# Kernel optimization log

Hardware: AMD Instinct MI355X
Metric: run time of the kernel (lower is better)

Reference implementation:

```python
import jax, jax.numpy as jnp
import numpy as np

T, H, E, I, K = 2048, 2048, 16, 512, 2
ROUTED_SCALE = 1.5   # config.moe_router_scaling_factor
SWIGLU_LIMIT = 7.0   # config.swiglu_limits[layer_id]


def setup_inputs() -> dict:
    key = jax.random.key(0)
    k1, k2, k3, k4, k5 = jax.random.split(key, 5)
    hidden_states = jax.random.normal(k1, (T, H), jnp.float32)
    gate_w = jax.random.normal(k2, (E, H), jnp.float32) * 0.02
    router_bias = jax.random.normal(k3, (E,), jnp.float32) * 0.01
    w13 = jax.random.normal(k4, (E, 2 * I, H), jnp.float32) * 0.02  # [gate; up] fused
    w2 = jax.random.normal(k5, (E, H, I), jnp.float32) * 0.02
    return {"hidden_states": hidden_states, "gate_w": gate_w,
            "router_bias": router_bias, "w13": w13, "w2": w2, "top_k": K}


def reference(hidden_states, gate_w, router_bias, w13, w2, top_k):
    n_tok = hidden_states.shape[0]
    n_exp = gate_w.shape[0]
    # fp32 gate (need_fp32_gate=True)
    router_logits = hidden_states.astype(jnp.float32) @ gate_w.T          # [T, E]
    scores = jax.nn.sigmoid(router_logits)
    # correction bias only affects expert choice, not the combine weights
    _, topk_ids = jax.lax.top_k(scores + router_bias[None, :], top_k)     # [T, K]
    topk_w = jnp.take_along_axis(scores, topk_ids, axis=1)                # [T, K]
    topk_w = topk_w / jnp.sum(topk_w, axis=1, keepdims=True)              # renormalize
    topk_w = topk_w * ROUTED_SCALE
    # scatter routing weights into dense per-expert combine weights [T, E]
    comb = jnp.zeros((n_tok, n_exp), jnp.float32)
    comb = comb.at[jnp.arange(n_tok)[:, None], topk_ids].add(topk_w)
    # expert SwiGLU MLPs, dense over experts (zero combine weight == not routed)
    gu = jnp.einsum('th,eoh->teo', hidden_states, w13)                    # [T, E, 2I]
    g, u = jnp.split(gu, 2, axis=-1)
    g = jnp.minimum(g, SWIGLU_LIMIT)                                      # gemm1_clamp_limit
    u = jnp.clip(u, -SWIGLU_LIMIT, SWIGLU_LIMIT)
    act = g * jax.nn.sigmoid(g) * u                                       # silu(gate) * up
    expert_out = jnp.einsum('tei,ehi->teh', act, w2)                      # [T, E, H]
    return jnp.einsum('teh,te->th', expert_out, comb)                     # [T, H]
```

## Files before the change

kernel.cpp:

```cpp
#include <hip/hip_runtime.h>
#include <hip/hip_bf16.h>
#include <math.h>

#define T_TOK 2048
#define H_DIM 2048
#define E_EXP 16
#define I_DIM 512
#define TWO_I 1024
#define ROUTED_SCALE 1.5f
#define SWIGLU_LIMIT 7.0f

#define BM 128
#define KC 64
#define MAX_TILES 48
#define PADMAX 6144

typedef __attribute__((ext_vector_type(8))) short bf16x8;
typedef __attribute__((ext_vector_type(4))) float f32x4;
typedef unsigned short u16;

__device__ inline u16 f2bf(float f) {
    return __builtin_bit_cast(u16, __float2bfloat16(f));
}
__device__ inline bf16x8 pack8(float4 a, float4 b) {
    bf16x8 v;
    v[0] = (short)f2bf(a.x); v[1] = (short)f2bf(a.y);
    v[2] = (short)f2bf(a.z); v[3] = (short)f2bf(a.w);
    v[4] = (short)f2bf(b.x); v[5] = (short)f2bf(b.y);
    v[6] = (short)f2bf(b.z); v[7] = (short)f2bf(b.w);
    return v;
}
__device__ inline ushort4 pack4(float4 a) {
    ushort4 v;
    v.x = f2bf(a.x); v.y = f2bf(a.y); v.z = f2bf(a.z); v.w = f2bf(a.w);
    return v;
}

__device__ inline void gload16(const u16* g, u16* l) {
    __builtin_amdgcn_global_load_lds(
        (const __attribute__((address_space(1))) void*)(g),
        (__attribute__((address_space(3))) void*)(l), 16, 0, 0);
}

#define SWZ(row, k) ((row) * 64 + ((k) ^ (((row) & 7) << 3)))

__global__ __launch_bounds__(256) void router_kernel(
    const float* __restrict__ hs, const float* __restrict__ gw,
    const float* __restrict__ bias, int* cnt, int* tok_list, float* w_list,
    u16* __restrict__ hs_bf)
{
    int wave = threadIdx.x >> 6;
    int lane = threadIdx.x & 63;
    int t = blockIdx.x * 4 + wave;
    if (t >= T_TOK) return;
    const float* x = hs + (size_t)t * H_DIM;

    float acc[E_EXP];
#pragma unroll
    for (int e = 0; e < E_EXP; ++e) acc[e] = 0.f;

#pragma unroll 2
    for (int c = 0; c < 8; ++c) {
        int col = c * 256 + lane * 4;
        float4 xv = *(const float4*)(x + col);
        *(ushort4*)(hs_bf + (size_t)t * H_DIM + col) = pack4(xv);
#pragma unroll
        for (int e = 0; e < E_EXP; ++e) {
            float4 gv = *(const float4*)(gw + (size_t)e * H_DIM + col);
            acc[e] = fmaf(xv.x, gv.x, acc[e]);
            acc[e] = fmaf(xv.y, gv.y, acc[e]);
            acc[e] = fmaf(xv.z, gv.z, acc[e]);
            acc[e] = fmaf(xv.w, gv.w, acc[e]);
        }
    }
#pragma unroll
    for (int e = 0; e < E_EXP; ++e) {
        for (int m = 32; m >= 1; m >>= 1)
            acc[e] += __shfl_xor(acc[e], m, 64);
    }
    if (lane == 0) {
        float sc[E_EXP], bsc[E_EXP];
#pragma unroll
        for (int e = 0; e < E_EXP; ++e) {
            sc[e] = 1.f / (1.f + expf(-acc[e]));
            bsc[e] = sc[e] + bias[e];
        }
        int e0 = 0; float b0 = bsc[0];
#pragma unroll
        for (int e = 1; e < E_EXP; ++e) if (bsc[e] > b0) { b0 = bsc[e]; e0 = e; }
        int e1 = -1; float b1 = -1e30f;
#pragma unroll
        for (int e = 0; e < E_EXP; ++e) {
            if (e == e0) continue;
            if (bsc[e] > b1) { b1 = bsc[e]; e1 = e; }
        }
        float s0 = sc[e0], s1 = sc[e1];
        float inv = ROUTED_SCALE / (s0 + s1);
        int p0 = atomicAdd(&cnt[e0], 1);
        tok_list[e0 * T_TOK + p0] = t;
        w_list[e0 * T_TOK + p0] = s0 * inv;
        int p1 = atomicAdd(&cnt[e1], 1);
        tok_list[e1 * T_TOK + p1] = t;
        w_list[e1 * T_TOK + p1] = s1 * inv;
    }
}

__global__ void scatter_build(const int* __restrict__ cnt,
    const int* __restrict__ tok_list, const float* __restrict__ w_list,
    int* A_tok, float* A_w, int* tile_e, int* tile_r0)
{
    int c[E_EXP], offs[E_EXP + 1];
    offs[0] = 0;
#pragma unroll
    for (int e = 0; e < E_EXP; ++e) {
        c[e] = cnt[e];
        offs[e + 1] = offs[e] + ((c[e] + BM - 1) & ~(BM - 1));
    }
    int idx = blockIdx.x * 256 + threadIdx.x;
    int e = idx >> 11;
    int pos = idx & (T_TOK - 1);
    int ce = c[e];
    int pe = (ce + BM - 1) & ~(BM - 1);
    if (pos < ce) {
        A_tok[offs[e] + pos] = tok_list[idx];
        A_w[offs[e] + pos] = w_list[idx];
    } else if (pos < pe) {
        A_tok[offs[e] + pos] = -1;
        A_w[offs[e] + pos] = 0.f;
    }
    if (idx == 0) {
        int nt = 0;
        for (int ee = 0; ee < E_EXP; ++ee) {
            int ntile = (c[ee] + BM - 1) >> 7;
            for (int j = 0; j < ntile; ++j) {
                tile_e[nt] = ee;
                tile_r0[nt] = offs[ee] + j * BM;
                ++nt;
            }
        }
        for (; nt < MAX_TILES; ++nt) tile_e[nt] = -1;
    }
}

__global__ __launch_bounds__(256, 2) void gemm1_act(
    const u16* __restrict__ hs_bf, const float* __restrict__ w13,
    const int* __restrict__ A_tok, const int* __restrict__ tile_e,
    const int* __restrict__ tile_r0, u16* __restrict__ act)
{
    int b = blockIdx.x;
    int id = (b & 7) * MAX_TILES + (b >> 3);
    int tile = id % MAX_TILES;
    int y = id / MAX_TILES;
    int e = tile_e[tile];
    if (e < 0) return;
    int row0 = tile_r0[tile];
    int i0 = y * 64;
    int tid = threadIdx.x;

    __shared__ u16 Xs[2][8192];
    __shared__ u16 Gs[2][4096];
    __shared__ u16 Us[2][4096];

    const int l = tid & 63, w = tid >> 6;

    const int rlo = l >> 3;
    const int c8 = (l & 7) << 3;
    const int ksrc = c8 ^ (rlo << 3);
    const u16* sX[4];
#pragma unroll
    for (int j = 0; j < 4; ++j) {
        int row = w * 32 + j * 8 + rlo;
        int tk = A_tok[row0 + row]; if (tk < 0) tk = 0;
        sX[j] = hs_bf + (size_t)tk * H_DIM + ksrc;
    }
    const int dX = w * 2048;

#define X_STAGE(bb, t) do { int ko = (t) * KC; \
    gload16(sX[0] + ko, &Xs[bb][dX]); \
    gload16(sX[1] + ko, &Xs[bb][dX + 512]); \
    gload16(sX[2] + ko, &Xs[bb][dX + 1024]); \
    gload16(sX[3] + ko, &Xs[bb][dX + 1536]); } while (0)

    const int srow = tid >> 2;
    const int c2 = tid & 3;
    const float* gsrc = w13 + ((size_t)e * TWO_I + i0 + srow) * H_DIM + c2 * 16;
    const float* usrc = gsrc + (size_t)I_DIM * H_DIM;
    const int wbA = SWZ(srow, c2 * 16);
    const int wbB = SWZ(srow, c2 * 16 + 8);

    float4 ga0, ga1, gb0, gb1, ua0, ua1, ub0, ub1;
#define W_LOAD(t) do { int k0 = (t) * KC; \
    ga0 = *(const float4*)(gsrc + k0);      ga1 = *(const float4*)(gsrc + k0 + 4); \
    gb0 = *(const float4*)(gsrc + k0 + 8);  gb1 = *(const float4*)(gsrc + k0 + 12); \
    ua0 = *(const float4*)(usrc + k0);      ua1 = *(const float4*)(usrc + k0 + 4); \
    ub0 = *(const float4*)(usrc + k0 + 8);  ub1 = *(const float4*)(usrc + k0 + 12); } while (0)

#define W_WRITE(bb) do { \
    *(bf16x8*)&Gs[bb][wbA] = pack8(ga0, ga1); \
    *(bf16x8*)&Gs[bb][wbB] = pack8(gb0, gb1); \
    *(bf16x8*)&Us[bb][wbA] = pack8(ua0, ua1); \
    *(bf16x8*)&Us[bb][wbB] = pack8(ub0, ub1); } while (0)

    const int wm = w >> 1, wn = w & 1;
    const int lr = l & 15, lg = l >> 4;
    int ia[4][2], ib[2][2];
#pragma unroll
    for (int kh = 0; kh < 2; ++kh) {
        int e2 = kh * 32 + lg * 8;
#pragma unroll
        for (int m = 0; m < 4; ++m) ia[m][kh] = SWZ(wm * 64 + m * 16 + lr, e2);
#pragma unroll
        for (int n = 0; n < 2; ++n) ib[n][kh] = SWZ(wn * 32 + n * 16 + lr, e2);
    }

    const f32x4 Z4 = {0.f, 0.f, 0.f, 0.f};
    f32x4 aG[4][2], aU[4][2];
#pragma unroll
    for (int m = 0; m < 4; ++m)
#pragma unroll
        for (int n = 0; n < 2; ++n) { aG[m][n] = Z4; aU[m][n] = Z4; }

    W_LOAD(0);
    X_STAGE(0, 0);
    W_WRITE(0);
    __syncthreads();
    int cur = 0;
    const int NT = H_DIM / KC;
    for (int t = 0; t < NT; ++t) {
        const bool more = (t + 1 < NT);
        if (more) {
            X_STAGE(cur ^ 1, t + 1);
            W_LOAD(t + 1);
            __builtin_amdgcn_sched_barrier(0);
        }
#pragma unroll
        for (int kh = 0; kh < 2; ++kh) {
            bf16x8 a0 = *(const bf16x8*)&Xs[cur][ia[0][kh]];
            bf16x8 a1 = *(const bf16x8*)&Xs[cur][ia[1][kh]];
            bf16x8 a2 = *(const bf16x8*)&Xs[cur][ia[2][kh]];
            bf16x8 a3 = *(const bf16x8*)&Xs[cur][ia[3][kh]];
            bf16x8 g0 = *(const bf16x8*)&Gs[cur][ib[0][kh]];
            bf16x8 g1 = *(const bf16x8*)&Gs[cur][ib[1][kh]];
            bf16x8 u0 = *(const bf16x8*)&Us[cur][ib[0][kh]];
            bf16x8 u1 = *(const bf16x8*)&Us[cur][ib[1][kh]];
            aG[0][0] = __builtin_amdgcn_mfma_f32_16x16x32_bf16(a0, g0, aG[0][0], 0, 0, 0);
            aG[0][1] = __builtin_amdgcn_mfma_f32_16x16x32_bf16(a0, g1, aG[0][1], 0, 0, 0);
            aG[1][0] = __builtin_amdgcn_mfma_f32_16x16x32_bf16(a1, g0, aG[1][0], 0, 0, 0);
            aG[1][1] = __builtin_amdgcn_mfma_f32_16x16x32_bf16(a1, g1, aG[1][1], 0, 0, 0);
            aG[2][0] = __builtin_amdgcn_mfma_f32_16x16x32_bf16(a2, g0, aG[2][0], 0, 0, 0);
            aG[2][1] = __builtin_amdgcn_mfma_f32_16x16x32_bf16(a2, g1, aG[2][1], 0, 0, 0);
            aG[3][0] = __builtin_amdgcn_mfma_f32_16x16x32_bf16(a3, g0, aG[3][0], 0, 0, 0);
            aG[3][1] = __builtin_amdgcn_mfma_f32_16x16x32_bf16(a3, g1, aG[3][1], 0, 0, 0);
            aU[0][0] = __builtin_amdgcn_mfma_f32_16x16x32_bf16(a0, u0, aU[0][0], 0, 0, 0);
            aU[0][1] = __builtin_amdgcn_mfma_f32_16x16x32_bf16(a0, u1, aU[0][1], 0, 0, 0);
            aU[1][0] = __builtin_amdgcn_mfma_f32_16x16x32_bf16(a1, u0, aU[1][0], 0, 0, 0);
            aU[1][1] = __builtin_amdgcn_mfma_f32_16x16x32_bf16(a1, u1, aU[1][1], 0, 0, 0);
            aU[2][0] = __builtin_amdgcn_mfma_f32_16x16x32_bf16(a2, u0, aU[2][0], 0, 0, 0);
            aU[2][1] = __builtin_amdgcn_mfma_f32_16x16x32_bf16(a2, u1, aU[2][1], 0, 0, 0);
            aU[3][0] = __builtin_amdgcn_mfma_f32_16x16x32_bf16(a3, u0, aU[3][0], 0, 0, 0);
            aU[3][1] = __builtin_amdgcn_mfma_f32_16x16x32_bf16(a3, u1, aU[3][1], 0, 0, 0);
        }
        if (more) W_WRITE(cur ^ 1);
        __syncthreads();
        cur ^= 1;
    }
#undef X_STAGE
#undef W_LOAD
#undef W_WRITE

#pragma unroll
    for (int m = 0; m < 4; ++m)
#pragma unroll
        for (int n = 0; n < 2; ++n) {
            int col = i0 + wn * 32 + n * 16 + lr;
            int rbase = row0 + wm * 64 + m * 16 + lg * 4;
#pragma unroll
            for (int q = 0; q < 4; ++q) {
                float g = fminf(aG[m][n][q], SWIGLU_LIMIT);
                float u = fminf(fmaxf(aU[m][n][q], -SWIGLU_LIMIT), SWIGLU_LIMIT);
                float s = 1.f / (1.f + __expf(-g));
                act[(size_t)(rbase + q) * I_DIM + col] = f2bf(g * s * u);
            }
        }
}

__global__ __launch_bounds__(256, 3) void gemm2_scatter(
    const u16* __restrict__ act, const float* __restrict__ w2,
    const int* __restrict__ A_tok, const float* __restrict__ A_w,
    const int* __restrict__ tile_e, const int* __restrict__ tile_r0,
    float* __restrict__ out)
{
    int b = blockIdx.x;
    int id = (b & 7) * 192 + (b >> 3);
    int tile = id % MAX_TILES;
    int y = id / MAX_TILES;
    int e = tile_e[tile];
    if (e < 0) return;
    int row0 = tile_r0[tile];
    int h0 = y * 64;
    int tid = threadIdx.x;

    __shared__ u16 As[2][8192];
    __shared__ u16 Bs[2][4096];
    __shared__ int toks[BM];
    __shared__ float wts[BM];
    if (tid < BM) { toks[tid] = A_tok[row0 + tid]; wts[tid] = A_w[row0 + tid]; }

    const int l = tid & 63, w = tid >> 6;

    const int rlo = l >> 3;
    const int c8 = (l & 7) << 3;
    const int ksrc = c8 ^ (rlo << 3);
    const u16* sA[4];
#pragma unroll
    for (int j = 0; j < 4; ++j) {
        int row = w * 32 + j * 8 + rlo;
        sA[j] = act + (size_t)(row0 + row) * I_DIM + ksrc;
    }
    const int dA = w * 2048;

#define A_STAGE(bb, t) do { int ko = (t) * KC; \
    gload16(sA[0] + ko, &As[bb][dA]); \
    gload16(sA[1] + ko, &As[bb][dA + 512]); \
    gload16(sA[2] + ko, &As[bb][dA + 1024]); \
    gload16(sA[3] + ko, &As[bb][dA + 1536]); } while (0)

    const int srow = tid >> 2;
    const int c2 = tid & 3;
    const float* bsrc = w2 + ((size_t)e * H_DIM + h0 + srow) * I_DIM + c2 * 16;
    const int wbA = SWZ(srow, c2 * 16);
    const int wbB = SWZ(srow, c2 * 16 + 8);

    float4 ba0, ba1, bb0, bb1;
#define B_LOAD(t) do { int k0 = (t) * KC; \
    ba0 = *(const float4*)(bsrc + k0);      ba1 = *(const float4*)(bsrc + k0 + 4); \
    bb0 = *(const float4*)(bsrc + k0 + 8);  bb1 = *(const float4*)(bsrc + k0 + 12); } while (0)

#define B_WRITE(bb) do { \
    *(bf16x8*)&Bs[bb][wbA] = pack8(ba0, ba1); \
    *(bf16x8*)&Bs[bb][wbB] = pack8(bb0, bb1); } while (0)

    const int wm = w >> 1, wn = w & 1;
    const int lr = l & 15, lg = l >> 4;
    int ia[4][2], ib[2][2];
#pragma unroll
    for (int kh = 0; kh < 2; ++kh) {
        int e2 = kh * 32 + lg * 8;
#pragma unroll
        for (int m = 0; m < 4; ++m) ia[m][kh] = SWZ(wm * 64 + m * 16 + lr, e2);
#pragma unroll
        for (int n = 0; n < 2; ++n) ib[n][kh] = SWZ(wn * 32 + n * 16 + lr, e2);
    }

    const f32x4 Z4 = {0.f, 0.f, 0.f, 0.f};
    f32x4 acc[4][2];
#pragma unroll
    for (int m = 0; m < 4; ++m)
#pragma unroll
        for (int n = 0; n < 2; ++n) acc[m][n] = Z4;

    B_LOAD(0);
    A_STAGE(0, 0);
    B_WRITE(0);
    __syncthreads();
    int cur = 0;
    const int NT = I_DIM / KC;
    for (int t = 0; t < NT; ++t) {
        const bool more = (t + 1 < NT);
        if (more) {
            A_STAGE(cur ^ 1, t + 1);
            B_LOAD(t + 1);
            __builtin_amdgcn_sched_barrier(0);
        }
#pragma unroll
        for (int kh = 0; kh < 2; ++kh) {
            bf16x8 a0 = *(const bf16x8*)&As[cur][ia[0][kh]];
            bf16x8 a1 = *(const bf16x8*)&As[cur][ia[1][kh]];
            bf16x8 a2 = *(const bf16x8*)&As[cur][ia[2][kh]];
            bf16x8 a3 = *(const bf16x8*)&As[cur][ia[3][kh]];
            bf16x8 b0 = *(const bf16x8*)&Bs[cur][ib[0][kh]];
            bf16x8 b1 = *(const bf16x8*)&Bs[cur][ib[1][kh]];
            acc[0][0] = __builtin_amdgcn_mfma_f32_16x16x32_bf16(a0, b0, acc[0][0], 0, 0, 0);
            acc[0][1] = __builtin_amdgcn_mfma_f32_16x16x32_bf16(a0, b1, acc[0][1], 0, 0, 0);
            acc[1][0] = __builtin_amdgcn_mfma_f32_16x16x32_bf16(a1, b0, acc[1][0], 0, 0, 0);
            acc[1][1] = __builtin_amdgcn_mfma_f32_16x16x32_bf16(a1, b1, acc[1][1], 0, 0, 0);
            acc[2][0] = __builtin_amdgcn_mfma_f32_16x16x32_bf16(a2, b0, acc[2][0], 0, 0, 0);
            acc[2][1] = __builtin_amdgcn_mfma_f32_16x16x32_bf16(a2, b1, acc[2][1], 0, 0, 0);
            acc[3][0] = __builtin_amdgcn_mfma_f32_16x16x32_bf16(a3, b0, acc[3][0], 0, 0, 0);
            acc[3][1] = __builtin_amdgcn_mfma_f32_16x16x32_bf16(a3, b1, acc[3][1], 0, 0, 0);
        }
        if (more) B_WRITE(cur ^ 1);
        __syncthreads();
        cur ^= 1;
    }
#undef A_STAGE
#undef B_LOAD
#undef B_WRITE

#pragma unroll
    for (int m = 0; m < 4; ++m)
#pragma unroll
        for (int n = 0; n < 2; ++n) {
            int col = h0 + wn * 32 + n * 16 + lr;
            int sbase = wm * 64 + m * 16 + lg * 4;
#pragma unroll
            for (int q = 0; q < 4; ++q) {
                int slot = sbase + q;
                int tok = toks[slot];
                if (tok >= 0)
                    atomicAdd(&out[(size_t)tok * H_DIM + col], acc[m][n][q] * wts[slot]);
            }
        }
}

extern "C" void kernel_launch(void* const* d_in, const int* in_sizes, int n_in,
                              void* d_out, int out_size, void* d_ws, size_t ws_size,
                              hipStream_t stream) {
    const float* hs   = (const float*)d_in[0];
    const float* gw   = (const float*)d_in[1];
    const float* bias = (const float*)d_in[2];
    const float* w13  = (const float*)d_in[3];
    const float* w2   = (const float*)d_in[4];
    float* out = (float*)d_out;

    char* ws = (char*)d_ws;
    int*   cnt      = (int*)(ws + 0);
    int*   tile_e   = (int*)(ws + 64);
    int*   tile_r0  = (int*)(ws + 320);
    int*   tok_list = (int*)(ws + 1024);
    float* w_list   = (float*)(ws + 132096);
    int*   A_tok    = (int*)(ws + 263168);
    float* A_w      = (float*)(ws + 287744);
    u16*   act      = (u16*)(ws + 315392);
    u16*   hs_bf    = (u16*)(ws + 6606848);

    hipMemsetAsync(d_out, 0, (size_t)T_TOK * H_DIM * sizeof(float), stream);
    hipMemsetAsync(cnt, 0, 64, stream);

    router_kernel<<<T_TOK / 4, 256, 0, stream>>>(hs, gw, bias, cnt, tok_list, w_list, hs_bf);
    scatter_build<<<(E_EXP * T_TOK) / 256, 256, 0, stream>>>(cnt, tok_list, w_list, A_tok, A_w, tile_e, tile_r0);

    gemm1_act<<<MAX_TILES * 8, 256, 0, stream>>>(hs_bf, w13, A_tok, tile_e, tile_r0, act);
    gemm2_scatter<<<MAX_TILES * 32, 256, 0, stream>>>(act, w2, A_tok, A_w, tile_e, tile_r0, out);
}
```

Baseline: 178.9 us.

## Stream fp32 weights directly into LDS via async loads and convert at MFMA read

Both expert GEMMs now bring the fp32 weight tiles into shared memory with global_load_lds instead of register loads followed by a bf16 pack and LDS store, and convert to bf16 when fragments are read. The K chunk is halved to 32 so the fp32 tiles fit, swizzles are redone, and the pipeline uses explicit vmcnt waits and raw barriers with two stages in flight. Launch-bound occupancy hints are raised, and gemm2 reads token ids and weights from global memory in the epilogue instead of shared memory. This removes register staging and VGPR pressure, at the cost of more loop iterations, more barriers, and duplicated conversion work across waves.

```diff
diff --git a/kernel.cpp b/kernel.cpp
--- a/kernel.cpp
+++ b/kernel.cpp
@@ -11,9 +11,8 @@
 #define SWIGLU_LIMIT 7.0f
 
 #define BM 128
-#define KC 64
+#define KC 32
 #define MAX_TILES 48
-#define PADMAX 6144
 
 typedef __attribute__((ext_vector_type(8))) short bf16x8;
 typedef __attribute__((ext_vector_type(4))) float f32x4;
@@ -21,28 +20,36 @@
 
 __device__ inline u16 f2bf(float f) {
     return __builtin_bit_cast(u16, __float2bfloat16(f));
-}
-__device__ inline bf16x8 pack8(float4 a, float4 b) {
-    bf16x8 v;
-    v[0] = (short)f2bf(a.x); v[1] = (short)f2bf(a.y);
-    v[2] = (short)f2bf(a.z); v[3] = (short)f2bf(a.w);
-    v[4] = (short)f2bf(b.x); v[5] = (short)f2bf(b.y);
-    v[6] = (short)f2bf(b.z); v[7] = (short)f2bf(b.w);
-    return v;
 }
 __device__ inline ushort4 pack4(float4 a) {
     ushort4 v;
     v.x = f2bf(a.x); v.y = f2bf(a.y); v.z = f2bf(a.z); v.w = f2bf(a.w);
     return v;
 }
+__device__ inline bf16x8 cvt8(f32x4 a, f32x4 b) {
+    bf16x8 v;
+    v[0] = (short)f2bf(a[0]); v[1] = (short)f2bf(a[1]);
+    v[2] = (short)f2bf(a[2]); v[3] = (short)f2bf(a[3]);
+    v[4] = (short)f2bf(b[0]); v[5] = (short)f2bf(b[1]);
+    v[6] = (short)f2bf(b[2]); v[7] = (short)f2bf(b[3]);
+    return v;
+}
 
 __device__ inline void gload16(const u16* g, u16* l) {
     __builtin_amdgcn_global_load_lds(
         (const __attribute__((address_space(1))) void*)(g),
         (__attribute__((address_space(3))) void*)(l), 16, 0, 0);
 }
-
-#define SWZ(row, k) ((row) * 64 + ((k) ^ (((row) & 7) << 3)))
+__device__ inline void gload16f(const float* g, float* l) {
+    __builtin_amdgcn_global_load_lds(
+        (const __attribute__((address_space(1))) void*)(g),
+        (__attribute__((address_space(3))) void*)(l), 16, 0, 0);
+}
+
+#define VM_WAIT(n) asm volatile("s_waitcnt vmcnt(" #n ")" ::: "memory")
+#define LGKM0()    asm volatile("s_waitcnt lgkmcnt(0)" ::: "memory")
+#define SBAR()     asm volatile("s_barrier" ::: "memory")
+#define SCHED0()   __builtin_amdgcn_sched_barrier(0)
 
 __global__ __launch_bounds__(256) void router_kernel(
     const float* __restrict__ hs, const float* __restrict__ gw,
@@ -142,7 +149,7 @@
     }
 }
 
-__global__ __launch_bounds__(256, 2) void gemm1_act(
+__global__ __launch_bounds__(256, 3) void gemm1_act(
     const u16* __restrict__ hs_bf, const float* __restrict__ w13,
     const int* __restrict__ A_tok, const int* __restrict__ tile_e,
     const int* __restrict__ tile_r0, u16* __restrict__ act)
@@ -157,60 +164,50 @@
     int i0 = y * 64;
     int tid = threadIdx.x;
 
-    __shared__ u16 Xs[2][8192];
-    __shared__ u16 Gs[2][4096];
-    __shared__ u16 Us[2][4096];
+    __shared__ u16  Xs[2][4096];
+    __shared__ float Gs[2][2048];
+    __shared__ float Us[2][2048];
 
     const int l = tid & 63, w = tid >> 6;
 
-    const int rlo = l >> 3;
-    const int c8 = (l & 7) << 3;
-    const int ksrc = c8 ^ (rlo << 3);
-    const u16* sX[4];
-#pragma unroll
-    for (int j = 0; j < 4; ++j) {
-        int row = w * 32 + j * 8 + rlo;
+    const u16* sX[2]; int dX[2];
+#pragma unroll
+    for (int j = 0; j < 2; ++j) {
+        int row = w * 32 + j * 16 + (l >> 2);
         int tk = A_tok[row0 + row]; if (tk < 0) tk = 0;
-        sX[j] = hs_bf + (size_t)tk * H_DIM + ksrc;
-    }
-    const int dX = w * 2048;
-
-#define X_STAGE(bb, t) do { int ko = (t) * KC; \
-    gload16(sX[0] + ko, &Xs[bb][dX]); \
-    gload16(sX[1] + ko, &Xs[bb][dX + 512]); \
-    gload16(sX[2] + ko, &Xs[bb][dX + 1024]); \
-    gload16(sX[3] + ko, &Xs[bb][dX + 1536]); } while (0)
-
-    const int srow = tid >> 2;
-    const int c2 = tid & 3;
-    const float* gsrc = w13 + ((size_t)e * TWO_I + i0 + srow) * H_DIM + c2 * 16;
-    const float* usrc = gsrc + (size_t)I_DIM * H_DIM;
-    const int wbA = SWZ(srow, c2 * 16);
-    const int wbB = SWZ(srow, c2 * 16 + 8);
-
-    float4 ga0, ga1, gb0, gb1, ua0, ua1, ub0, ub1;
-#define W_LOAD(t) do { int k0 = (t) * KC; \
-    ga0 = *(const float4*)(gsrc + k0);      ga1 = *(const float4*)(gsrc + k0 + 4); \
-    gb0 = *(const float4*)(gsrc + k0 + 8);  gb1 = *(const float4*)(gsrc + k0 + 12); \
-    ua0 = *(const float4*)(usrc + k0);      ua1 = *(const float4*)(usrc + k0 + 4); \
-    ub0 = *(const float4*)(usrc + k0 + 8);  ub1 = *(const float4*)(usrc + k0 + 12); } while (0)
-
-#define W_WRITE(bb) do { \
-    *(bf16x8*)&Gs[bb][wbA] = pack8(ga0, ga1); \
-    *(bf16x8*)&Gs[bb][wbB] = pack8(gb0, gb1); \
-    *(bf16x8*)&Us[bb][wbA] = pack8(ua0, ua1); \
-    *(bf16x8*)&Us[bb][wbB] = pack8(ub0, ub1); } while (0)
+        int sg = (l & 3) ^ ((l >> 3) & 3);
+        sX[j] = hs_bf + (size_t)tk * H_DIM + sg * 8;
+        dX[j] = (w * 32 + j * 16) * 32;
+    }
+    const float* sG[2]; const float* sU[2]; int dW[2];
+#pragma unroll
+    for (int j = 0; j < 2; ++j) {
+        int row = w * 16 + j * 8 + (l >> 3);
+        int sg = (l & 7) ^ (l >> 3);
+        sG[j] = w13 + ((size_t)e * TWO_I + i0 + row) * H_DIM + sg * 4;
+        sU[j] = sG[j] + (size_t)I_DIM * H_DIM;
+        dW[j] = (w * 16 + j * 8) * 32;
+    }
+
+#define G1_ISSUE(bb, t) do { int ko = (t) * KC; \
+    gload16(sX[0] + ko, &Xs[bb][dX[0]]);  gload16(sX[1] + ko, &Xs[bb][dX[1]]); \
+    gload16f(sG[0] + ko, &Gs[bb][dW[0]]); gload16f(sG[1] + ko, &Gs[bb][dW[1]]); \
+    gload16f(sU[0] + ko, &Us[bb][dW[0]]); gload16f(sU[1] + ko, &Us[bb][dW[1]]); \
+    SCHED0(); } while (0)
 
     const int wm = w >> 1, wn = w & 1;
     const int lr = l & 15, lg = l >> 4;
-    int ia[4][2], ib[2][2];
-#pragma unroll
-    for (int kh = 0; kh < 2; ++kh) {
-        int e2 = kh * 32 + lg * 8;
-#pragma unroll
-        for (int m = 0; m < 4; ++m) ia[m][kh] = SWZ(wm * 64 + m * 16 + lr, e2);
-#pragma unroll
-        for (int n = 0; n < 2; ++n) ib[n][kh] = SWZ(wn * 32 + n * 16 + lr, e2);
+    int ix[4], ig[2][2];
+#pragma unroll
+    for (int m = 0; m < 4; ++m) {
+        int ra = wm * 64 + m * 16 + lr;
+        ix[m] = ra * 32 + (lg ^ ((lr >> 1) & 3)) * 8;
+    }
+#pragma unroll
+    for (int n = 0; n < 2; ++n) {
+        int rb = wn * 32 + n * 16 + lr;
+        ig[n][0] = rb * 32 + ((lg * 2)     ^ (lr & 7)) * 4;
+        ig[n][1] = rb * 32 + ((lg * 2 + 1) ^ (lr & 7)) * 4;
     }
 
     const f32x4 Z4 = {0.f, 0.f, 0.f, 0.f};
@@ -220,53 +217,42 @@
 #pragma unroll
         for (int n = 0; n < 2; ++n) { aG[m][n] = Z4; aU[m][n] = Z4; }
 
-    W_LOAD(0);
-    X_STAGE(0, 0);
-    W_WRITE(0);
-    __syncthreads();
+#define G1_MFMA(c) do { \
+    bf16x8 xa[4], gg[2], uu[2]; \
+    _Pragma("unroll") for (int m = 0; m < 4; ++m) xa[m] = *(const bf16x8*)&Xs[c][ix[m]]; \
+    _Pragma("unroll") for (int n = 0; n < 2; ++n) { \
+        f32x4 q0 = *(const f32x4*)&Gs[c][ig[n][0]]; \
+        f32x4 q1 = *(const f32x4*)&Gs[c][ig[n][1]]; \
+        gg[n] = cvt8(q0, q1); \
+        f32x4 r0 = *(const f32x4*)&Us[c][ig[n][0]]; \
+        f32x4 r1 = *(const f32x4*)&Us[c][ig[n][1]]; \
+        uu[n] = cvt8(r0, r1); } \
+    _Pragma("unroll") for (int m = 0; m < 4; ++m) \
+    _Pragma("unroll") for (int n = 0; n < 2; ++n) { \
+        aG[m][n] = __builtin_amdgcn_mfma_f32_16x16x32_bf16(xa[m], gg[n], aG[m][n], 0, 0, 0); \
+        aU[m][n] = __builtin_amdgcn_mfma_f32_16x16x32_bf16(xa[m], uu[n], aU[m][n], 0, 0, 0); } \
+    } while (0)
+
+    const int NT = H_DIM / KC;
+    G1_ISSUE(0, 0);
+    G1_ISSUE(1, 1);
     int cur = 0;
-    const int NT = H_DIM / KC;
-    for (int t = 0; t < NT; ++t) {
-        const bool more = (t + 1 < NT);
-        if (more) {
-            X_STAGE(cur ^ 1, t + 1);
-            W_LOAD(t + 1);
-            __builtin_amdgcn_sched_barrier(0);
-        }
-#pragma unroll
-        for (int kh = 0; kh < 2; ++kh) {
-            bf16x8 a0 = *(const bf16x8*)&Xs[cur][ia[0][kh]];
-            bf16x8 a1 = *(const bf16x8*)&Xs[cur][ia[1][kh]];
-            bf16x8 a2 = *(const bf16x8*)&Xs[cur][ia[2][kh]];
-            bf16x8 a3 = *(const bf16x8*)&Xs[cur][ia[3][kh]];
-            bf16x8 g0 = *(const bf16x8*)&Gs[cur][ib[0][kh]];
-            bf16x8 g1 = *(const bf16x8*)&Gs[cur][ib[1][kh]];
-            bf16x8 u0 = *(const bf16x8*)&Us[cur][ib[0][kh]];
-            bf16x8 u1 = *(const bf16x8*)&Us[cur][ib[1][kh]];
-            aG[0][0] = __builtin_amdgcn_mfma_f32_16x16x32_bf16(a0, g0, aG[0][0], 0, 0, 0);
-            aG[0][1] = __builtin_amdgcn_mfma_f32_16x16x32_bf16(a0, g1, aG[0][1], 0, 0, 0);
-            aG[1][0] = __builtin_amdgcn_mfma_f32_16x16x32_bf16(a1, g0, aG[1][0], 0, 0, 0);
-            aG[1][1] = __builtin_amdgcn_mfma_f32_16x16x32_bf16(a1, g1, aG[1][1], 0, 0, 0);
-            aG[2][0] = __builtin_amdgcn_mfma_f32_16x16x32_bf16(a2, g0, aG[2][0], 0, 0, 0);
-            aG[2][1] = __builtin_amdgcn_mfma_f32_16x16x32_bf16(a2, g1, aG[2][1], 0, 0, 0);
-            aG[3][0] = __builtin_amdgcn_mfma_f32_16x16x32_bf16(a3, g0, aG[3][0], 0, 0, 0);
-            aG[3][1] = __builtin_amdgcn_mfma_f32_16x16x32_bf16(a3, g1, aG[3][1], 0, 0, 0);
-            aU[0][0] = __builtin_amdgcn_mfma_f32_16x16x32_bf16(a0, u0, aU[0][0], 0, 0, 0);
-            aU[0][1] = __builtin_amdgcn_mfma_f32_16x16x32_bf16(a0, u1, aU[0][1], 0, 0, 0);
-            aU[1][0] = __builtin_amdgcn_mfma_f32_16x16x32_bf16(a1, u0, aU[1][0], 0, 0, 0);
-            aU[1][1] = __builtin_amdgcn_mfma_f32_16x16x32_bf16(a1, u1, aU[1][1], 0, 0, 0);
-            aU[2][0] = __builtin_amdgcn_mfma_f32_16x16x32_bf16(a2, u0, aU[2][0], 0, 0, 0);
-            aU[2][1] = __builtin_amdgcn_mfma_f32_16x16x32_bf16(a2, u1, aU[2][1], 0, 0, 0);
-            aU[3][0] = __builtin_amdgcn_mfma_f32_16x16x32_bf16(a3, u0, aU[3][0], 0, 0, 0);
-            aU[3][1] = __builtin_amdgcn_mfma_f32_16x16x32_bf16(a3, u1, aU[3][1], 0, 0, 0);
-        }
-        if (more) W_WRITE(cur ^ 1);
-        __syncthreads();
+    for (int t = 0; t < NT - 1; ++t) {
+        VM_WAIT(6);
+        SBAR();
+        G1_MFMA(cur);
+        if (t + 2 < NT) {
+            LGKM0();
+            SBAR();
+            G1_ISSUE(cur, t + 2);
+        }
         cur ^= 1;
     }
-#undef X_STAGE
-#undef W_LOAD
-#undef W_WRITE
+    VM_WAIT(0);
+    SBAR();
+    G1_MFMA(cur);
+#undef G1_ISSUE
+#undef G1_MFMA
 
 #pragma unroll
     for (int m = 0; m < 4; ++m)
@@ -284,7 +270,7 @@
         }
 }
 
-__global__ __launch_bounds__(256, 3) void gemm2_scatter(
+__global__ __launch_bounds__(256, 4) void gemm2_scatter(
     const u16* __restrict__ act, const float* __restrict__ w2,
     const int* __restrict__ A_tok, const float* __restrict__ A_w,
     const int* __restrict__ tile_e, const int* __restrict__ tile_r0,
@@ -300,56 +286,46 @@
     int h0 = y * 64;
     int tid = threadIdx.x;
 
-    __shared__ u16 As[2][8192];
-    __shared__ u16 Bs[2][4096];
-    __shared__ int toks[BM];
-    __shared__ float wts[BM];
-    if (tid < BM) { toks[tid] = A_tok[row0 + tid]; wts[tid] = A_w[row0 + tid]; }
+    __shared__ u16  As[2][4096];
+    __shared__ float Bs[2][2048];
 
     const int l = tid & 63, w = tid >> 6;
 
-    const int rlo = l >> 3;
-    const int c8 = (l & 7) << 3;
-    const int ksrc = c8 ^ (rlo << 3);
-    const u16* sA[4];
-#pragma unroll
-    for (int j = 0; j < 4; ++j) {
-        int row = w * 32 + j * 8 + rlo;
-        sA[j] = act + (size_t)(row0 + row) * I_DIM + ksrc;
-    }
-    const int dA = w * 2048;
-
-#define A_STAGE(bb, t) do { int ko = (t) * KC; \
-    gload16(sA[0] + ko, &As[bb][dA]); \
-    gload16(sA[1] + ko, &As[bb][dA + 512]); \
-    gload16(sA[2] + ko, &As[bb][dA + 1024]); \
-    gload16(sA[3] + ko, &As[bb][dA + 1536]); } while (0)
-
-    const int srow = tid >> 2;
-    const int c2 = tid & 3;
-    const float* bsrc = w2 + ((size_t)e * H_DIM + h0 + srow) * I_DIM + c2 * 16;
-    const int wbA = SWZ(srow, c2 * 16);
-    const int wbB = SWZ(srow, c2 * 16 + 8);
-
-    float4 ba0, ba1, bb0, bb1;
-#define B_LOAD(t) do { int k0 = (t) * KC; \
-    ba0 = *(const float4*)(bsrc + k0);      ba1 = *(const float4*)(bsrc + k0 + 4); \
-    bb0 = *(const float4*)(bsrc + k0 + 8);  bb1 = *(const float4*)(bsrc + k0 + 12); } while (0)
-
-#define B_WRITE(bb) do { \
-    *(bf16x8*)&Bs[bb][wbA] = pack8(ba0, ba1); \
-    *(bf16x8*)&Bs[bb][wbB] = pack8(bb0, bb1); } while (0)
+    const u16* sA[2]; int dA[2];
+#pragma unroll
+    for (int j = 0; j < 2; ++j) {
+        int row = w * 32 + j * 16 + (l >> 2);
+        int sg = (l & 3) ^ ((l >> 3) & 3);
+        sA[j] = act + (size_t)(row0 + row) * I_DIM + sg * 8;
+        dA[j] = (w * 32 + j * 16) * 32;
+    }
+    const float* sB[2]; int dB[2];
+#pragma unroll
+    for (int j = 0; j < 2; ++j) {
+        int row = w * 16 + j * 8 + (l >> 3);
+        int sg = (l & 7) ^ (l >> 3);
+        sB[j] = w2 + ((size_t)e * H_DIM + h0 + row) * I_DIM + sg * 4;
+        dB[j] = (w * 16 + j * 8) * 32;
+    }
+
+#define G2_ISSUE(bb, t) do { int ko = (t) * KC; \
+    gload16(sA[0] + ko, &As[bb][dA[0]]);  gload16(sA[1] + ko, &As[bb][dA[1]]); \
+    gload16f(sB[0] + ko, &Bs[bb][dB[0]]); gload16f(sB[1] + ko, &Bs[bb][dB[1]]); \
+    SCHED0(); } while (0)
 
     const int wm = w >> 1, wn = w & 1;
     const int lr = l & 15, lg = l >> 4;
-    int ia[4][2], ib[2][2];
-#pragma unroll
-    for (int kh = 0; kh < 2; ++kh) {
-        int e2 = kh * 32 + lg * 8;
-#pragma unroll
-        for (int m = 0; m < 4; ++m) ia[m][kh] = SWZ(wm * 64 + m * 16 + lr, e2);
-#pragma unroll
-        for (int n = 0; n < 2; ++n) ib[n][kh] = SWZ(wn * 32 + n * 16 + lr, e2);
+    int ix[4], ig[2][2];
+#pragma unroll
+    for (int m = 0; m < 4; ++m) {
+        int ra = wm * 64 + m * 16 + lr;
+        ix[m] = ra * 32 + (lg ^ ((lr >> 1) & 3)) * 8;
+    }
+#pragma unroll
+    for (int n = 0; n < 2; ++n) {
+        int rb = wn * 32 + n * 16 + lr;
+        ig[n][0] = rb * 32 + ((lg * 2)     ^ (lr & 7)) * 4;
+        ig[n][1] = rb * 32 + ((lg * 2 + 1) ^ (lr & 7)) * 4;
     }
 
     const f32x4 Z4 = {0.f, 0.f, 0.f, 0.f};
@@ -359,43 +335,38 @@
 #pragma unroll
         for (int n = 0; n < 2; ++n) acc[m][n] = Z4;
 
-    B_LOAD(0);
-    A_STAGE(0, 0);
-    B_WRITE(0);
-    __syncthreads();
+#define G2_MFMA(c) do { \
+    bf16x8 xa[4], bb2[2]; \
+    _Pragma("unroll") for (int m = 0; m < 4; ++m) xa[m] = *(const bf16x8*)&As[c][ix[m]]; \
+    _Pragma("unroll") for (int n = 0; n < 2; ++n) { \
+        f32x4 q0 = *(const f32x4*)&Bs[c][ig[n][0]]; \
+        f32x4 q1 = *(const f32x4*)&Bs[c][ig[n][1]]; \
+        bb2[n] = cvt8(q0, q1); } \
+    _Pragma("unroll") for (int m = 0; m < 4; ++m) \
+    _Pragma("unroll") for (int n = 0; n < 2; ++n) \
+        acc[m][n] = __builtin_amdgcn_mfma_f32_16x16x32_bf16(xa[m], bb2[n], acc[m][n], 0, 0, 0); \
+    } while (0)
+
+    const int NT = I_DIM / KC;
+    G2_ISSUE(0, 0);
+    G2_ISSUE(1, 1);
     int cur = 0;
-    const int NT = I_DIM / KC;
-    for (int t = 0; t < NT; ++t) {
-        const bool more = (t + 1 < NT);
-        if (more) {
-            A_STAGE(cur ^ 1, t + 1);
-            B_LOAD(t + 1);
-            __builtin_amdgcn_sched_barrier(0);
-        }
-#pragma unroll
-        for (int kh = 0; kh < 2; ++kh) {
-            bf16x8 a0 = *(const bf16x8*)&As[cur][ia[0][kh]];
-            bf16x8 a1 = *(const bf16x8*)&As[cur][ia[1][kh]];
-            bf16x8 a2 = *(const bf16x8*)&As[cur][ia[2][kh]];
-            bf16x8 a3 = *(const bf16x8*)&As[cur][ia[3][kh]];
-            bf16x8 b0 = *(const bf16x8*)&Bs[cur][ib[0][kh]];
-            bf16x8 b1 = *(const bf16x8*)&Bs[cur][ib[1][kh]];
-            acc[0][0] = __builtin_amdgcn_mfma_f32_16x16x32_bf16(a0, b0, acc[0][0], 0, 0, 0);
-            acc[0][1] = __builtin_amdgcn_mfma_f32_16x16x32_bf16(a0, b1, acc[0][1], 0, 0, 0);
-            acc[1][0] = __builtin_amdgcn_mfma_f32_16x16x32_bf16(a1, b0, acc[1][0], 0, 0, 0);
-            acc[1][1] = __builtin_amdgcn_mfma_f32_16x16x32_bf16(a1, b1, acc[1][1], 0, 0, 0);
-            acc[2][0] = __builtin_amdgcn_mfma_f32_16x16x32_bf16(a2, b0, acc[2][0], 0, 0, 0);
-            acc[2][1] = __builtin_amdgcn_mfma_f32_16x16x32_bf16(a2, b1, acc[2][1], 0, 0, 0);
-            acc[3][0] = __builtin_amdgcn_mfma_f32_16x16x32_bf16(a3, b0, acc[3][0], 0, 0, 0);
-            acc[3][1] = __builtin_amdgcn_mfma_f32_16x16x32_bf16(a3, b1, acc[3][1], 0, 0, 0);
-        }
-        if (more) B_WRITE(cur ^ 1);
-        __syncthreads();
+    for (int t = 0; t < NT - 1; ++t) {
+        VM_WAIT(4);
+        SBAR();
+        G2_MFMA(cur);
+        if (t + 2 < NT) {
+            LGKM0();
+            SBAR();
+            G2_ISSUE(cur, t + 2);
+        }
         cur ^= 1;
     }
-#undef A_STAGE
-#undef B_LOAD
-#undef B_WRITE
+    VM_WAIT(0);
+    SBAR();
+    G2_MFMA(cur);
+#undef G2_ISSUE
+#undef G2_MFMA
 
 #pragma unroll
     for (int m = 0; m < 4; ++m)
@@ -405,10 +376,10 @@
             int sbase = wm * 64 + m * 16 + lg * 4;
 #pragma unroll
             for (int q = 0; q < 4; ++q) {
-                int slot = sbase + q;
-                int tok = toks[slot];
+                int slot = row0 + sbase + q;
+                int tok = A_tok[slot];
                 if (tok >= 0)
-                    atomicAdd(&out[(size_t)tok * H_DIM + col], acc[m][n][q] * wts[slot]);
+                    atomicAdd(&out[(size_t)tok * H_DIM + col], acc[m][n][q] * A_w[slot]);
             }
         }
 }
```

Result: slower. 201.9 us (+12.8%).

## Split-K gemm1 with separate SwiGLU pass and wider gemm2 tiles

Applied to the files above, without the earlier changes.

Gemm1 now splits the hidden dimension into two halves across blocks, writing fp32 gate/up partials to a workspace buffer. A new elementwise kernel sums the partials and applies clamp plus SiLU to produce bf16 activations. KC is halved to 32 with a new swizzle, and gemm2 gets 128-wide H tiles with a 4x4 MFMA grid per wave. The split doubles gemm1 parallelism, which previously had only 384 blocks. In exchange it adds an extra launch and a large fp32 partial write and read of about 50MB, and halves work per barrier.

```diff
diff --git a/kernel.cpp b/kernel.cpp
--- a/kernel.cpp
+++ b/kernel.cpp
@@ -11,9 +11,9 @@
 #define SWIGLU_LIMIT 7.0f
 
 #define BM 128
-#define KC 64
+#define KC 32
 #define MAX_TILES 48
-#define PADMAX 6144
+#define SLOTS 6144
 
 typedef __attribute__((ext_vector_type(8))) short bf16x8;
 typedef __attribute__((ext_vector_type(4))) float f32x4;
@@ -22,7 +22,12 @@
 __device__ inline u16 f2bf(float f) {
     return __builtin_bit_cast(u16, __float2bfloat16(f));
 }
-__device__ inline bf16x8 pack8(float4 a, float4 b) {
+__device__ inline ushort4 pack4(float4 a) {
+    ushort4 v;
+    v.x = f2bf(a.x); v.y = f2bf(a.y); v.z = f2bf(a.z); v.w = f2bf(a.w);
+    return v;
+}
+__device__ inline bf16x8 cvt8(float4 a, float4 b) {
     bf16x8 v;
     v[0] = (short)f2bf(a.x); v[1] = (short)f2bf(a.y);
     v[2] = (short)f2bf(a.z); v[3] = (short)f2bf(a.w);
@@ -30,19 +35,13 @@
     v[6] = (short)f2bf(b.z); v[7] = (short)f2bf(b.w);
     return v;
 }
-__device__ inline ushort4 pack4(float4 a) {
-    ushort4 v;
-    v.x = f2bf(a.x); v.y = f2bf(a.y); v.z = f2bf(a.z); v.w = f2bf(a.w);
-    return v;
-}
 
 __device__ inline void gload16(const u16* g, u16* l) {
     __builtin_amdgcn_global_load_lds(
         (const __attribute__((address_space(1))) void*)(g),
         (__attribute__((address_space(3))) void*)(l), 16, 0, 0);
 }
-
-#define SWZ(row, k) ((row) * 64 + ((k) ^ (((row) & 7) << 3)))
+#define SCHED0() __builtin_amdgcn_sched_barrier(0)
 
 __global__ __launch_bounds__(256) void router_kernel(
     const float* __restrict__ hs, const float* __restrict__ gw,
@@ -142,76 +141,63 @@
     }
 }
 
-__global__ __launch_bounds__(256, 2) void gemm1_act(
+__global__ __launch_bounds__(256, 3) void gemm1_gu(
     const u16* __restrict__ hs_bf, const float* __restrict__ w13,
     const int* __restrict__ A_tok, const int* __restrict__ tile_e,
-    const int* __restrict__ tile_r0, u16* __restrict__ act)
+    const int* __restrict__ tile_r0, float* __restrict__ gu_part)
 {
     int b = blockIdx.x;
-    int id = (b & 7) * MAX_TILES + (b >> 3);
-    int tile = id % MAX_TILES;
-    int y = id / MAX_TILES;
+    int y = b & 7;
+    int kspl = (b >> 3) & 1;
+    int tile = b >> 4;
     int e = tile_e[tile];
     if (e < 0) return;
     int row0 = tile_r0[tile];
     int i0 = y * 64;
+    int k0base = kspl * (H_DIM / 2);
     int tid = threadIdx.x;
 
-    __shared__ u16 Xs[2][8192];
-    __shared__ u16 Gs[2][4096];
-    __shared__ u16 Us[2][4096];
+    __shared__ u16 Xs[2][4096];
+    __shared__ u16 Gs[2][2048];
+    __shared__ u16 Us[2][2048];
 
     const int l = tid & 63, w = tid >> 6;
 
-    const int rlo = l >> 3;
-    const int c8 = (l & 7) << 3;
-    const int ksrc = c8 ^ (rlo << 3);
-    const u16* sX[4];
-#pragma unroll
-    for (int j = 0; j < 4; ++j) {
-        int row = w * 32 + j * 8 + rlo;
+    const u16* sX[2]; int dX[2];
+#pragma unroll
+    for (int j = 0; j < 2; ++j) {
+        int row = w * 32 + j * 16 + (l >> 2);
         int tk = A_tok[row0 + row]; if (tk < 0) tk = 0;
-        sX[j] = hs_bf + (size_t)tk * H_DIM + ksrc;
-    }
-    const int dX = w * 2048;
-
+        int sg = (l & 3) ^ ((l >> 3) & 3);
+        sX[j] = hs_bf + (size_t)tk * H_DIM + k0base + sg * 8;
+        dX[j] = (w * 32 + j * 16) * 32;
+    }
 #define X_STAGE(bb, t) do { int ko = (t) * KC; \
-    gload16(sX[0] + ko, &Xs[bb][dX]); \
-    gload16(sX[1] + ko, &Xs[bb][dX + 512]); \
-    gload16(sX[2] + ko, &Xs[bb][dX + 1024]); \
-    gload16(sX[3] + ko, &Xs[bb][dX + 1536]); } while (0)
-
-    const int srow = tid >> 2;
-    const int c2 = tid & 3;
-    const float* gsrc = w13 + ((size_t)e * TWO_I + i0 + srow) * H_DIM + c2 * 16;
+    gload16(sX[0] + ko, &Xs[bb][dX[0]]); gload16(sX[1] + ko, &Xs[bb][dX[1]]); } while (0)
+
+    const int wr = tid >> 2;
+    const int wg = tid & 3;
+    const int wsk = (wg ^ ((wr >> 1) & 3)) * 8;
+    const float* gsrc = w13 + ((size_t)e * TWO_I + i0 + wr) * H_DIM + k0base + wsk;
     const float* usrc = gsrc + (size_t)I_DIM * H_DIM;
-    const int wbA = SWZ(srow, c2 * 16);
-    const int wbB = SWZ(srow, c2 * 16 + 8);
-
-    float4 ga0, ga1, gb0, gb1, ua0, ua1, ub0, ub1;
-#define W_LOAD(t) do { int k0 = (t) * KC; \
-    ga0 = *(const float4*)(gsrc + k0);      ga1 = *(const float4*)(gsrc + k0 + 4); \
-    gb0 = *(const float4*)(gsrc + k0 + 8);  gb1 = *(const float4*)(gsrc + k0 + 12); \
-    ua0 = *(const float4*)(usrc + k0);      ua1 = *(const float4*)(usrc + k0 + 4); \
-    ub0 = *(const float4*)(usrc + k0 + 8);  ub1 = *(const float4*)(usrc + k0 + 12); } while (0)
-
+    const int wdst = wr * 32 + wg * 8;
+
+    float4 gA, gB, uA, uB;
+#define W_LOAD(t) do { int ko = (t) * KC; \
+    gA = *(const float4*)(gsrc + ko); gB = *(const float4*)(gsrc + ko + 4); \
+    uA = *(const float4*)(usrc + ko); uB = *(const float4*)(usrc + ko + 4); } while (0)
 #define W_WRITE(bb) do { \
-    *(bf16x8*)&Gs[bb][wbA] = pack8(ga0, ga1); \
-    *(bf16x8*)&Gs[bb][wbB] = pack8(gb0, gb1); \
-    *(bf16x8*)&Us[bb][wbA] = pack8(ua0, ua1); \
-    *(bf16x8*)&Us[bb][wbB] = pack8(ub0, ub1); } while (0)
+    *(bf16x8*)&Gs[bb][wdst] = cvt8(gA, gB); \
+    *(bf16x8*)&Us[bb][wdst] = cvt8(uA, uB); } while (0)
 
     const int wm = w >> 1, wn = w & 1;
     const int lr = l & 15, lg = l >> 4;
-    int ia[4][2], ib[2][2];
-#pragma unroll
-    for (int kh = 0; kh < 2; ++kh) {
-        int e2 = kh * 32 + lg * 8;
-#pragma unroll
-        for (int m = 0; m < 4; ++m) ia[m][kh] = SWZ(wm * 64 + m * 16 + lr, e2);
-#pragma unroll
-        for (int n = 0; n < 2; ++n) ib[n][kh] = SWZ(wn * 32 + n * 16 + lr, e2);
-    }
+    const int swz = (lg ^ ((lr >> 1) & 3)) * 8;
+    int ix[4], ib[2];
+#pragma unroll
+    for (int m = 0; m < 4; ++m) ix[m] = (wm * 64 + m * 16 + lr) * 32 + swz;
+#pragma unroll
+    for (int n = 0; n < 2; ++n) ib[n] = (wn * 32 + n * 16 + lr) * 32 + swz;
 
     const f32x4 Z4 = {0.f, 0.f, 0.f, 0.f};
     f32x4 aG[4][2], aU[4][2];
@@ -225,24 +211,23 @@
     W_WRITE(0);
     __syncthreads();
     int cur = 0;
-    const int NT = H_DIM / KC;
+    const int NT = (H_DIM / 2) / KC;
     for (int t = 0; t < NT; ++t) {
         const bool more = (t + 1 < NT);
         if (more) {
             X_STAGE(cur ^ 1, t + 1);
             W_LOAD(t + 1);
-            __builtin_amdgcn_sched_barrier(0);
-        }
-#pragma unroll
-        for (int kh = 0; kh < 2; ++kh) {
-            bf16x8 a0 = *(const bf16x8*)&Xs[cur][ia[0][kh]];
-            bf16x8 a1 = *(const bf16x8*)&Xs[cur][ia[1][kh]];
-            bf16x8 a2 = *(const bf16x8*)&Xs[cur][ia[2][kh]];
-            bf16x8 a3 = *(const bf16x8*)&Xs[cur][ia[3][kh]];
-            bf16x8 g0 = *(const bf16x8*)&Gs[cur][ib[0][kh]];
-            bf16x8 g1 = *(const bf16x8*)&Gs[cur][ib[1][kh]];
-            bf16x8 u0 = *(const bf16x8*)&Us[cur][ib[0][kh]];
-            bf16x8 u1 = *(const bf16x8*)&Us[cur][ib[1][kh]];
+            SCHED0();
+        }
+        {
+            bf16x8 a0 = *(const bf16x8*)&Xs[cur][ix[0]];
+            bf16x8 a1 = *(const bf16x8*)&Xs[cur][ix[1]];
+            bf16x8 a2 = *(const bf16x8*)&Xs[cur][ix[2]];
+            bf16x8 a3 = *(const bf16x8*)&Xs[cur][ix[3]];
+            bf16x8 g0 = *(const bf16x8*)&Gs[cur][ib[0]];
+            bf16x8 g1 = *(const bf16x8*)&Gs[cur][ib[1]];
+            bf16x8 u0 = *(const bf16x8*)&Us[cur][ib[0]];
+            bf16x8 u1 = *(const bf16x8*)&Us[cur][ib[1]];
             aG[0][0] = __builtin_amdgcn_mfma_f32_16x16x32_bf16(a0, g0, aG[0][0], 0, 0, 0);
             aG[0][1] = __builtin_amdgcn_mfma_f32_16x16x32_bf16(a0, g1, aG[0][1], 0, 0, 0);
             aG[1][0] = __builtin_amdgcn_mfma_f32_16x16x32_bf16(a1, g0, aG[1][0], 0, 0, 0);
@@ -268,20 +253,55 @@
 #undef W_LOAD
 #undef W_WRITE
 
+    float* gp = gu_part + (size_t)kspl * SLOTS * TWO_I;
 #pragma unroll
     for (int m = 0; m < 4; ++m)
 #pragma unroll
         for (int n = 0; n < 2; ++n) {
             int col = i0 + wn * 32 + n * 16 + lr;
-            int rbase = row0 + wm * 64 + m * 16 + lg * 4;
+            int sbase = row0 + wm * 64 + m * 16 + lg * 4;
 #pragma unroll
             for (int q = 0; q < 4; ++q) {
-                float g = fminf(aG[m][n][q], SWIGLU_LIMIT);
-                float u = fminf(fmaxf(aU[m][n][q], -SWIGLU_LIMIT), SWIGLU_LIMIT);
-                float s = 1.f / (1.f + __expf(-g));
-                act[(size_t)(rbase + q) * I_DIM + col] = f2bf(g * s * u);
+                gp[(size_t)(sbase + q) * TWO_I + col]         = aG[m][n][q];
+                gp[(size_t)(sbase + q) * TWO_I + I_DIM + col] = aU[m][n][q];
             }
         }
+}
+
+__global__ __launch_bounds__(256) void swiglu_pass(
+    const float* __restrict__ gu_part, u16* __restrict__ act)
+{
+    int idx = blockIdx.x * 256 + threadIdx.x;
+    int slot = idx >> 7;
+    int i4 = (idx & 127) << 2;
+    const float* p0 = gu_part + (size_t)slot * TWO_I + i4;
+    const float* p1 = p0 + (size_t)SLOTS * TWO_I;
+    float4 g0 = *(const float4*)p0;
+    float4 g1 = *(const float4*)p1;
+    float4 u0 = *(const float4*)(p0 + I_DIM);
+    float4 u1 = *(const float4*)(p1 + I_DIM);
+    float4 r;
+    {
+        float g = fminf(g0.x + g1.x, SWIGLU_LIMIT);
+        float u = fminf(fmaxf(u0.x + u1.x, -SWIGLU_LIMIT), SWIGLU_LIMIT);
+        r.x = g * (1.f / (1.f + __expf(-g))) * u;
+    }
+    {
+        float g = fminf(g0.y + g1.y, SWIGLU_LIMIT);
+        float u = fminf(fmaxf(u0.y + u1.y, -SWIGLU_LIMIT), SWIGLU_LIMIT);
+        r.y = g * (1.f / (1.f + __expf(-g))) * u;
+    }
+    {
+        float g = fminf(g0.z + g1.z, SWIGLU_LIMIT);
+        float u = fminf(fmaxf(u0.z + u1.z, -SWIGLU_LIMIT), SWIGLU_LIMIT);
+        r.z = g * (1.f / (1.f + __expf(-g))) * u;
+    }
+    {
+        float g = fminf(g0.w + g1.w, SWIGLU_LIMIT);
+        float u = fminf(fmaxf(u0.w + u1.w, -SWIGLU_LIMIT), SWIGLU_LIMIT);
+        r.w = g * (1.f / (1.f + __expf(-g))) * u;
+    }
+    *(ushort4*)(act + (size_t)slot * I_DIM + i4) = pack4(r);
 }
 
 __global__ __launch_bounds__(256, 3) void gemm2_scatter(
@@ -291,73 +311,60 @@
     float* __restrict__ out)
 {
     int b = blockIdx.x;
-    int id = (b & 7) * 192 + (b >> 3);
-    int tile = id % MAX_TILES;
-    int y = id / MAX_TILES;
+    int y = (b & 7) * 2 + ((b >> 3) & 1);
+    int tile = b >> 4;
     int e = tile_e[tile];
     if (e < 0) return;
     int row0 = tile_r0[tile];
-    int h0 = y * 64;
+    int h0 = y * 128;
     int tid = threadIdx.x;
 
-    __shared__ u16 As[2][8192];
+    __shared__ u16 As[2][4096];
     __shared__ u16 Bs[2][4096];
-    __shared__ int toks[BM];
-    __shared__ float wts[BM];
-    if (tid < BM) { toks[tid] = A_tok[row0 + tid]; wts[tid] = A_w[row0 + tid]; }
 
     const int l = tid & 63, w = tid >> 6;
 
-    const int rlo = l >> 3;
-    const int c8 = (l & 7) << 3;
-    const int ksrc = c8 ^ (rlo << 3);
-    const u16* sA[4];
-#pragma unroll
-    for (int j = 0; j < 4; ++j) {
-        int row = w * 32 + j * 8 + rlo;
-        sA[j] = act + (size_t)(row0 + row) * I_DIM + ksrc;
-    }
-    const int dA = w * 2048;
-
+    const u16* sA[2]; int dA[2];
+#pragma unroll
+    for (int j = 0; j < 2; ++j) {
+        int row = w * 32 + j * 16 + (l >> 2);
+        int sg = (l & 3) ^ ((l >> 3) & 3);
+        sA[j] = act + (size_t)(row0 + row) * I_DIM + sg * 8;
+        dA[j] = (w * 32 + j * 16) * 32;
+    }
 #define A_STAGE(bb, t) do { int ko = (t) * KC; \
-    gload16(sA[0] + ko, &As[bb][dA]); \
-    gload16(sA[1] + ko, &As[bb][dA + 512]); \
-    gload16(sA[2] + ko, &As[bb][dA + 1024]); \
-    gload16(sA[3] + ko, &As[bb][dA + 1536]); } while (0)
-
-    const int srow = tid >> 2;
-    const int c2 = tid & 3;
-    const float* bsrc = w2 + ((size_t)e * H_DIM + h0 + srow) * I_DIM + c2 * 16;
-    const int wbA = SWZ(srow, c2 * 16);
-    const int wbB = SWZ(srow, c2 * 16 + 8);
-
-    float4 ba0, ba1, bb0, bb1;
-#define B_LOAD(t) do { int k0 = (t) * KC; \
-    ba0 = *(const float4*)(bsrc + k0);      ba1 = *(const float4*)(bsrc + k0 + 4); \
-    bb0 = *(const float4*)(bsrc + k0 + 8);  bb1 = *(const float4*)(bsrc + k0 + 12); } while (0)
-
+    gload16(sA[0] + ko, &As[bb][dA[0]]); gload16(sA[1] + ko, &As[bb][dA[1]]); } while (0)
+
+    const int wr = tid >> 1;
+    const int wg0 = (tid & 1) * 2;
+    const float* bsrc = w2 + ((size_t)e * H_DIM + h0 + wr) * I_DIM;
+    const int sk0 = ((wg0)     ^ ((wr >> 1) & 3)) * 8;
+    const int sk1 = ((wg0 + 1) ^ ((wr >> 1) & 3)) * 8;
+    const int wd0 = wr * 32 + wg0 * 8;
+
+    float4 b0a, b0b, b1a, b1b;
+#define B_LOAD(t) do { int ko = (t) * KC; \
+    b0a = *(const float4*)(bsrc + ko + sk0); b0b = *(const float4*)(bsrc + ko + sk0 + 4); \
+    b1a = *(const float4*)(bsrc + ko + sk1); b1b = *(const float4*)(bsrc + ko + sk1 + 4); } while (0)
 #define B_WRITE(bb) do { \
-    *(bf16x8*)&Bs[bb][wbA] = pack8(ba0, ba1); \
-    *(bf16x8*)&Bs[bb][wbB] = pack8(bb0, bb1); } while (0)
+    *(bf16x8*)&Bs[bb][wd0]     = cvt8(b0a, b0b); \
+    *(bf16x8*)&Bs[bb][wd0 + 8] = cvt8(b1a, b1b); } while (0)
 
     const int wm = w >> 1, wn = w & 1;
     const int lr = l & 15, lg = l >> 4;
-    int ia[4][2], ib[2][2];
-#pragma unroll
-    for (int kh = 0; kh < 2; ++kh) {
-        int e2 = kh * 32 + lg * 8;
-#pragma unroll
-        for (int m = 0; m < 4; ++m) ia[m][kh] = SWZ(wm * 64 + m * 16 + lr, e2);
-#pragma unroll
-        for (int n = 0; n < 2; ++n) ib[n][kh] = SWZ(wn * 32 + n * 16 + lr, e2);
-    }
+    const int swz = (lg ^ ((lr >> 1) & 3)) * 8;
+    int ix[4], ib[4];
+#pragma unroll
+    for (int m = 0; m < 4; ++m) ix[m] = (wm * 64 + m * 16 + lr) * 32 + swz;
+#pragma unroll
+    for (int n = 0; n < 4; ++n) ib[n] = (wn * 64 + n * 16 + lr) * 32 + swz;
 
     const f32x4 Z4 = {0.f, 0.f, 0.f, 0.f};
-    f32x4 acc[4][2];
+    f32x4 acc[4][4];
 #pragma unroll
     for (int m = 0; m < 4; ++m)
 #pragma unroll
-        for (int n = 0; n < 2; ++n) acc[m][n] = Z4;
+        for (int n = 0; n < 4; ++n) acc[m][n] = Z4;
 
     B_LOAD(0);
     A_STAGE(0, 0);
@@ -370,24 +377,19 @@
         if (more) {
             A_STAGE(cur ^ 1, t + 1);
             B_LOAD(t + 1);
-            __builtin_amdgcn_sched_barrier(0);
-        }
-#pragma unroll
-        for (int kh = 0; kh < 2; ++kh) {
-            bf16x8 a0 = *(const bf16x8*)&As[cur][ia[0][kh]];
-            bf16x8 a1 = *(const bf16x8*)&As[cur][ia[1][kh]];
-            bf16x8 a2 = *(const bf16x8*)&As[cur][ia[2][kh]];
-            bf16x8 a3 = *(const bf16x8*)&As[cur][ia[3][kh]];
-            bf16x8 b0 = *(const bf16x8*)&Bs[cur][ib[0][kh]];
-            bf16x8 b1 = *(const bf16x8*)&Bs[cur][ib[1][kh]];
-            acc[0][0] = __builtin_amdgcn_mfma_f32_16x16x32_bf16(a0, b0, acc[0][0], 0, 0, 0);
-            acc[0][1] = __builtin_amdgcn_mfma_f32_16x16x32_bf16(a0, b1, acc[0][1], 0, 0, 0);
-            acc[1][0] = __builtin_amdgcn_mfma_f32_16x16x32_bf16(a1, b0, acc[1][0], 0, 0, 0);
-            acc[1][1] = __builtin_amdgcn_mfma_f32_16x16x32_bf16(a1, b1, acc[1][1], 0, 0, 0);
-            acc[2][0] = __builtin_amdgcn_mfma_f32_16x16x32_bf16(a2, b0, acc[2][0], 0, 0, 0);
-            acc[2][1] = __builtin_amdgcn_mfma_f32_16x16x32_bf16(a2, b1, acc[2][1], 0, 0, 0);
-            acc[3][0] = __builtin_amdgcn_mfma_f32_16x16x32_bf16(a3, b0, acc[3][0], 0, 0, 0);
-            acc[3][1] = __builtin_amdgcn_mfma_f32_16x16x32_bf16(a3, b1, acc[3][1], 0, 0, 0);
+            SCHED0();
+        }
+        {
+            bf16x8 a[4], bb[4];
+#pragma unroll
+            for (int m = 0; m < 4; ++m) a[m] = *(const bf16x8*)&As[cur][ix[m]];
+#pragma unroll
+            for (int n = 0; n < 4; ++n) bb[n] = *(const bf16x8*)&Bs[cur][ib[n]];
+#pragma unroll
+            for (int m = 0; m < 4; ++m)
+#pragma unroll
+                for (int n = 0; n < 4; ++n)
+                    acc[m][n] = __builtin_amdgcn_mfma_f32_16x16x32_bf16(a[m], bb[n], acc[m][n], 0, 0, 0);
         }
         if (more) B_WRITE(cur ^ 1);
         __syncthreads();
@@ -400,15 +402,15 @@
 #pragma unroll
     for (int m = 0; m < 4; ++m)
 #pragma unroll
-        for (int n = 0; n < 2; ++n) {
-            int col = h0 + wn * 32 + n * 16 + lr;
-            int sbase = wm * 64 + m * 16 + lg * 4;
+        for (int n = 0; n < 4; ++n) {
+            int col = h0 + wn * 64 + n * 16 + lr;
+            int sbase = row0 + wm * 64 + m * 16 + lg * 4;
 #pragma unroll
             for (int q = 0; q < 4; ++q) {
                 int slot = sbase + q;
-                int tok = toks[slot];
+                int tok = A_tok[slot];
                 if (tok >= 0)
-                    atomicAdd(&out[(size_t)tok * H_DIM + col], acc[m][n][q] * wts[slot]);
+                    atomicAdd(&out[(size_t)tok * H_DIM + col], acc[m][n][q] * A_w[slot]);
             }
         }
 }
@@ -433,6 +435,7 @@
     float* A_w      = (float*)(ws + 287744);
     u16*   act      = (u16*)(ws + 315392);
     u16*   hs_bf    = (u16*)(ws + 6606848);
+    float* gu_part  = (float*)(ws + 14995456);
 
     hipMemsetAsync(d_out, 0, (size_t)T_TOK * H_DIM * sizeof(float), stream);
     hipMemsetAsync(cnt, 0, 64, stream);
@@ -440,6 +443,7 @@
     router_kernel<<<T_TOK / 4, 256, 0, stream>>>(hs, gw, bias, cnt, tok_list, w_list, hs_bf);
     scatter_build<<<(E_EXP * T_TOK) / 256, 256, 0, stream>>>(cnt, tok_list, w_list, A_tok, A_w, tile_e, tile_r0);
 
-    gemm1_act<<<MAX_TILES * 8, 256, 0, stream>>>(hs_bf, w13, A_tok, tile_e, tile_r0, act);
-    gemm2_scatter<<<MAX_TILES * 32, 256, 0, stream>>>(act, w2, A_tok, A_w, tile_e, tile_r0, out);
-}
+    gemm1_gu<<<MAX_TILES * 8 * 2, 256, 0, stream>>>(hs_bf, w13, A_tok, tile_e, tile_r0, gu_part);
+    swiglu_pass<<<SLOTS * I_DIM / 4 / 256, 256, 0, stream>>>(gu_part, act);
+    gemm2_scatter<<<MAX_TILES * 16, 256, 0, stream>>>(act, w2, A_tok, A_w, tile_e, tile_r0, out);
+}
```

Result: slower. 209.3 us (+17.0%).
